# Performance work log

Hardware: AMD Instinct MI355X
Metric: run time of the kernel (lower is better)

Reference implementation:

```python
import jax, jax.numpy as jnp
import numpy as np

HEADS = 8
DIM_HEAD = 64


def setup_inputs() -> dict:
    key = jax.random.key(0)
    k1, k2, k3 = jax.random.split(key, 3)
    dim = 512
    hidden = HEADS * DIM_HEAD  # 512
    x = jax.random.normal(k1, (16, dim, 64, 64), dtype=jnp.float32)
    # 1x1 convs are matmuls over channels; store weights as [out_ch, in_ch]
    w_qkv = jax.random.normal(k2, (3 * hidden, dim), dtype=jnp.float32) * (1.0 / np.sqrt(dim))
    w_out = jax.random.normal(k3, (dim, hidden), dtype=jnp.float32) * (1.0 / np.sqrt(hidden))
    b_out = jnp.zeros((dim,), dtype=jnp.float32)
    return {"x": x, "w_qkv": w_qkv, "w_out": w_out, "b_out": b_out}


def reference(x, w_qkv, w_out, b_out):
    b, c, h, w = x.shape
    n = h * w
    xf = x.reshape(b, c, n)                          # [b, c, n]
    qkv = jnp.einsum('oc,bcn->bon', w_qkv, xf)        # 1x1 conv, no bias -> [b, 3*H*D, n]
    qkv = qkv.reshape(b, 3, HEADS, DIM_HEAD, n)       # split (qkv heads c)
    q, k, v = qkv[:, 0], qkv[:, 1], qkv[:, 2]         # each [b, H, D, n]
    k = jax.nn.softmax(k, axis=-1)                    # softmax over spatial tokens
    context = jnp.einsum('bhdn,bhen->bhde', k, v)     # [b, H, D, D]
    out = jnp.einsum('bhde,bhdn->bhen', context, q)   # [b, H, D, n]
    out = out.reshape(b, HEADS * DIM_HEAD, n)
    out = jnp.einsum('oc,bcn->bon', w_out, out) + b_out[None, :, None]  # 1x1 conv + bias
    return out.reshape(b, -1, h, w)
```

## Files before the change

### kernel.cpp

```cpp
#include <hip/hip_runtime.h>
#include <hip/hip_bf16.h>
#include <math.h>


typedef __attribute__((ext_vector_type(8))) __bf16 bf16x8;
typedef __attribute__((ext_vector_type(4))) float f32x4;

__device__ inline void async_ld16(const void* g, void* s) {
    __builtin_amdgcn_global_load_lds(
        (const __attribute__((address_space(1))) void*)g,
        (__attribute__((address_space(3))) void*)s, 16, 0, 0);
}

template<bool OUTBF, bool BIAS>
__global__ __launch_bounds__(256) void gemm_mfma(
    const __bf16* __restrict__ A, const __bf16* __restrict__ BT,
    void* __restrict__ Cv, const float* __restrict__ bias,
    int K, int N, long aBS, long bBS, long cBS)
{
    __shared__ __bf16 As[128 * 32];
    __shared__ __bf16 Bs[128 * 32];

    const int t = threadIdx.x;
    const int lane = t & 63, wv = t >> 6;
    const int z = blockIdx.z;
    const int row0 = blockIdx.y * 128, col0 = blockIdx.x * 128;

    A  += (long)z * aBS;
    BT += (long)z * bBS;

    const int wm = (wv >> 1) * 64, wn = (wv & 1) * 64;
    const int lr = lane & 15, kg = lane >> 4;

    f32x4 acc[4][4] = {};

    const int srow = (lane >> 2);
    const int skk  = (lane & 3) * 8;

    for (int k0 = 0; k0 < K; k0 += 32) {
        #pragma unroll
        for (int it = 0; it < 2; it++) {
            int c = it * 4 + wv;
            int r = c * 16 + srow;
            async_ld16(A  + (long)(row0 + r) * K + k0 + skk, &As[c * 512 + lane * 8]);
            async_ld16(BT + (long)(col0 + r) * K + k0 + skk, &Bs[c * 512 + lane * 8]);
        }
        __syncthreads();

        bf16x8 af[4], bfr[4];
        #pragma unroll
        for (int i = 0; i < 4; i++) {
            af[i]  = *(const bf16x8*)&As[(wm + i * 16 + lr) * 32 + kg * 8];
            bfr[i] = *(const bf16x8*)&Bs[(wn + i * 16 + lr) * 32 + kg * 8];
        }
        #pragma unroll
        for (int i = 0; i < 4; i++)
            #pragma unroll
            for (int j = 0; j < 4; j++)
                acc[i][j] = __builtin_amdgcn_mfma_f32_16x16x32_bf16(af[i], bfr[j], acc[i][j], 0, 0, 0);
        __syncthreads();
    }

    #pragma unroll
    for (int i = 0; i < 4; i++) {
        #pragma unroll
        for (int j = 0; j < 4; j++) {
            #pragma unroll
            for (int r = 0; r < 4; r++) {
                int row = row0 + wm + i * 16 + kg * 4 + r;
                int col = col0 + wn + j * 16 + lr;
                float v = acc[i][j][r];
                if (OUTBF) {
                    ((__hip_bfloat16*)Cv)[(long)z * cBS + (long)row * N + col] = __float2bfloat16(v);
                } else {
                    if (BIAS) v += bias[row];
                    ((float*)Cv)[(long)z * cBS + (long)row * N + col] = v;
                }
            }
        }
    }
}

__global__ __launch_bounds__(256) void transpose_cast(
    const float* __restrict__ x, __hip_bfloat16* __restrict__ xT)
{
    __shared__ float tile[32][33];
    int z = blockIdx.z;
    int n0 = blockIdx.x * 32, c0 = blockIdx.y * 32;
    int tx = threadIdx.x & 31, ty = threadIdx.x >> 5;

    const float* xb = x + (long)z * 512 * 4096;
    #pragma unroll
    for (int i = 0; i < 4; i++)
        tile[ty + i * 8][tx] = xb[(long)(c0 + ty + i * 8) * 4096 + n0 + tx];
    __syncthreads();

    __hip_bfloat16* xTb = xT + (long)z * 4096 * 512;
    #pragma unroll
    for (int i = 0; i < 4; i++) {
        int nl = ty + i * 8;
        xTb[(long)(n0 + nl) * 512 + c0 + tx] = __float2bfloat16(tile[tx][nl]);
    }
}

__global__ __launch_bounds__(256) void cast_bf(
    const float* __restrict__ in, __hip_bfloat16* __restrict__ out, int n)
{
    for (int i = blockIdx.x * 256 + threadIdx.x; i < n; i += gridDim.x * 256)
        out[i] = __float2bfloat16(in[i]);
}

__global__ __launch_bounds__(256) void softmax_bf(__hip_bfloat16* __restrict__ kv)
{
    int b = blockIdx.x >> 9;
    int r = blockIdx.x & 511;
    unsigned short* row = (unsigned short*)(kv + ((long)b * 1024 + r) * 4096);

    int t = threadIdx.x, lane = t & 63, wv = t >> 6;
    __shared__ float red[8];

    float vals[16];
    float m = -INFINITY;
    #pragma unroll
    for (int i = 0; i < 2; i++) {
        uint4 raw = *(const uint4*)&row[8 * t + 2048 * i];
        unsigned v[4] = {raw.x, raw.y, raw.z, raw.w};
        #pragma unroll
        for (int j = 0; j < 4; j++) {
            float lo = __uint_as_float(v[j] << 16);
            float hi = __uint_as_float(v[j] & 0xffff0000u);
            vals[i * 8 + j * 2]     = lo;
            vals[i * 8 + j * 2 + 1] = hi;
            m = fmaxf(m, fmaxf(lo, hi));
        }
    }
    #pragma unroll
    for (int off = 32; off > 0; off >>= 1) m = fmaxf(m, __shfl_down(m, off));
    if (lane == 0) red[wv] = m;
    __syncthreads();
    if (t == 0) red[0] = fmaxf(fmaxf(red[0], red[1]), fmaxf(red[2], red[3]));
    __syncthreads();
    m = red[0];

    float s = 0.0f;
    #pragma unroll
    for (int i = 0; i < 16; i++) { vals[i] = __expf(vals[i] - m); s += vals[i]; }
    #pragma unroll
    for (int off = 32; off > 0; off >>= 1) s += __shfl_down(s, off);
    if (lane == 0) red[4 + wv] = s;
    __syncthreads();
    if (t == 0) red[4] = red[4] + red[5] + red[6] + red[7];
    __syncthreads();
    float inv = 1.0f / red[4];

    #pragma unroll
    for (int i = 0; i < 2; i++) {
        unsigned v[4];
        #pragma unroll
        for (int j = 0; j < 4; j++) {
            __hip_bfloat16 lo = __float2bfloat16(vals[i * 8 + j * 2] * inv);
            __hip_bfloat16 hi = __float2bfloat16(vals[i * 8 + j * 2 + 1] * inv);
            v[j] = (unsigned)(*(unsigned short*)&lo) | ((unsigned)(*(unsigned short*)&hi) << 16);
        }
        uint4 o; o.x = v[0]; o.y = v[1]; o.z = v[2]; o.w = v[3];
        *(uint4*)&row[8 * t + 2048 * i] = o;
    }
}

template<bool BF16>
__device__ inline float ldg_cvt(const float* p, long i) {
    if (BF16) return __bfloat162float(((const __hip_bfloat16*)p)[i]);
    return p[i];
}

template<bool TRANSB, bool BIAS, int MODE, bool BF16IN>
__global__ __launch_bounds__(256) void gemm64(
    const float* __restrict__ A, const float* __restrict__ Bm,
    float* __restrict__ Cm, const float* __restrict__ bias,
    int M, int Nn, int K, int ldA, int ldB, int ldC,
    long aBS, long bBS, long cBS)
{
    const int t  = threadIdx.x;
    const int tx = t & 15;
    const int ty = t >> 4;
    const int z  = blockIdx.z;

    int row0 = blockIdx.y * 64;
    int col0 = blockIdx.x * 64;

    long aBase = 0, bBase = 0, cBase = 0;
    if (MODE == 0) {
        aBase = z * aBS; bBase = z * bBS; cBase = z * cBS;
    } else if (MODE == 1) {
        int bh = z >> 3, ks = z & 7;
        int b = bh >> 3, h = bh & 7;
        aBase = ((long)b * 1024 + h * 64) * 4096 + ks * 512;
        bBase = ((long)b * 1024 + 512 + h * 64) * 4096 + ks * 512;
        cBase = (long)z * 4096;
    } else {
        aBase = (long)(z & 7) * 64;
        bBase = (long)z * 4096;
        cBase = (long)(z >> 3) * 262144 + (long)(z & 7) * 64;
    }

    __shared__ __align__(16) float As[16][68];
    __shared__ __align__(16) float Bs[16][68];

    float acc[4][4] = {};

    for (int k0 = 0; k0 < K; k0 += 16) {
        {
            int k = t & 15, r = t >> 4;
            #pragma unroll
            for (int i = 0; i < 4; i++)
                As[k][r + i * 16] = ldg_cvt<BF16IN>(A, aBase + (long)(row0 + r + i * 16) * ldA + k0 + k);
        }
        if (TRANSB) {
            int k = t & 15, c = t >> 4;
            #pragma unroll
            for (int i = 0; i < 4; i++)
                Bs[k][c + i * 16] = ldg_cvt<BF16IN>(Bm, bBase + (long)(col0 + c + i * 16) * ldB + k0 + k);
        } else {
            int c = t & 63, kq = t >> 6;
            #pragma unroll
            for (int i = 0; i < 4; i++)
                Bs[kq + i * 4][c] = ldg_cvt<BF16IN>(Bm, bBase + (long)(k0 + kq + i * 4) * ldB + col0 + c);
        }
        __syncthreads();

        #pragma unroll
        for (int kk = 0; kk < 16; kk++) {
            float4 a4 = *(const float4*)&As[kk][ty * 4];
            float4 b4 = *(const float4*)&Bs[kk][tx * 4];
            float av[4] = {a4.x, a4.y, a4.z, a4.w};
            float bv[4] = {b4.x, b4.y, b4.z, b4.w};
            #pragma unroll
            for (int i = 0; i < 4; i++)
                #pragma unroll
                for (int j = 0; j < 4; j++)
                    acc[i][j] = fmaf(av[i], bv[j], acc[i][j]);
        }
        __syncthreads();
    }

    #pragma unroll
    for (int i = 0; i < 4; i++) {
        int r = row0 + ty * 4 + i;
        float bv = BIAS ? bias[r] : 0.0f;
        float4 o;
        o.x = acc[i][0] + bv; o.y = acc[i][1] + bv;
        o.z = acc[i][2] + bv; o.w = acc[i][3] + bv;
        *(float4*)&Cm[cBase + (long)r * ldC + col0 + tx * 4] = o;
    }
}

__global__ __launch_bounds__(256) void reduce_ctx(
    const float* __restrict__ part, float* __restrict__ ctx)
{
    int bh = blockIdx.x;
    for (int i = threadIdx.x; i < 4096; i += 256) {
        float s = 0.0f;
        #pragma unroll
        for (int ks = 0; ks < 8; ks++)
            s += part[((long)bh * 8 + ks) * 4096 + i];
        ctx[(long)bh * 4096 + i] = s;
    }
}

extern "C" void kernel_launch(void* const* d_in, const int* in_sizes, int n_in,
                              void* d_out, int out_size, void* d_ws, size_t ws_size,
                              hipStream_t stream)
{
    const float* x     = (const float*)d_in[0];
    const float* w_qkv = (const float*)d_in[1];
    const float* w_out = (const float*)d_in[2];
    const float* b_out = (const float*)d_in[3];
    float* out = (float*)d_out;

    char* ws = (char*)d_ws;
    __hip_bfloat16* kv_bf  = (__hip_bfloat16*)(ws);
    __hip_bfloat16* xT     = (__hip_bfloat16*)(ws + 134217728L);
    float*          ctxp   = (float*)(ws + 201326592L);
    float*          ctx    = (float*)(ws + 218103808L);
    float*          w2     = (float*)(ws + 220200960L);
    float*          w3     = (float*)(ws + 236978176L);
    __hip_bfloat16* w3bf   = (__hip_bfloat16*)(ws + 253755392L);
    __hip_bfloat16* wkvbf  = (__hip_bfloat16*)(ws + 262144000L);

    transpose_cast<<<dim3(128, 16, 16), 256, 0, stream>>>(x, xT);
    cast_bf<<<dim3(512), 256, 0, stream>>>(w_qkv + 512 * 512, wkvbf, 1024 * 512);

    gemm_mfma<true, false><<<dim3(32, 8, 16), 256, 0, stream>>>(
        (const __bf16*)wkvbf, (const __bf16*)xT, kv_bf, nullptr,
        512, 4096, 0L, (long)4096 * 512, (long)1024 * 4096);

    softmax_bf<<<dim3(8192), 256, 0, stream>>>(kv_bf);

    gemm64<true, false, 1, true><<<dim3(1, 1, 1024), 256, 0, stream>>>(
        (const float*)kv_bf, (const float*)kv_bf, ctxp, nullptr,
        64, 64, 512, 4096, 4096, 64, 0L, 0L, 0L);
    reduce_ctx<<<dim3(128), 256, 0, stream>>>(ctxp, ctx);

    gemm64<true, false, 2, false><<<dim3(1, 8, 128), 256, 0, stream>>>(
        w_out, ctx, w2, nullptr,
        512, 64, 64, 512, 64, 512, 0L, 0L, 0L);

    gemm64<false, false, 0, false><<<dim3(8, 8, 16), 256, 0, stream>>>(
        w2, w_qkv, w3, nullptr,
        512, 512, 512, 512, 512, 512,
        262144L, 0L, 262144L);
    cast_bf<<<dim3(512), 256, 0, stream>>>(w3, w3bf, 16 * 512 * 512);

    gemm_mfma<false, true><<<dim3(32, 4, 16), 256, 0, stream>>>(
        (const __bf16*)w3bf, (const __bf16*)xT, out, b_out,
        512, 4096, (long)512 * 512, (long)4096 * 512, (long)512 * 4096);
}
```

Baseline: 584.8 us.

## Fuse softmax normalization into MFMA context kernel and move weight-fold GEMM to MFMA

Splits the softmax into a row-stats pass that writes only max and inverse sum. The exp and normalization are then recomputed inside a new MFMA-based context kernel, which removes the write-back of normalized K. The scalar fp32 w2·w_qkv fold GEMM is replaced by a bf16 MFMA GEMM using a transposed bf16 copy of the Q weights, and its output is written as bf16 directly, dropping the separate cast pass. This adds an extra weight transpose kernel and recomputes exp once per element. It also lowers the precision of the intermediate w2 and w3.

```diff
diff --git a/kernel.cpp b/kernel.cpp
--- a/kernel.cpp
+++ b/kernel.cpp
@@ -103,6 +103,21 @@
     }
 }
 
+__global__ __launch_bounds__(256) void transpose_cast_sq(
+    const float* __restrict__ in, __hip_bfloat16* __restrict__ out)
+{
+    __shared__ float tile[32][33];
+    int r0 = blockIdx.y * 32, c0 = blockIdx.x * 32;
+    int tx = threadIdx.x & 31, ty = threadIdx.x >> 5;
+    #pragma unroll
+    for (int i = 0; i < 4; i++)
+        tile[ty + i * 8][tx] = in[(long)(r0 + ty + i * 8) * 512 + c0 + tx];
+    __syncthreads();
+    #pragma unroll
+    for (int i = 0; i < 4; i++)
+        out[(long)(c0 + ty + i * 8) * 512 + r0 + tx] = __float2bfloat16(tile[tx][ty + i * 8]);
+}
+
 __global__ __launch_bounds__(256) void cast_bf(
     const float* __restrict__ in, __hip_bfloat16* __restrict__ out, int n)
 {
@@ -110,11 +125,12 @@
         out[i] = __float2bfloat16(in[i]);
 }
 
-__global__ __launch_bounds__(256) void softmax_bf(__hip_bfloat16* __restrict__ kv)
+__global__ __launch_bounds__(256) void row_stats(
+    const __hip_bfloat16* __restrict__ kv, float2* __restrict__ stats)
 {
     int b = blockIdx.x >> 9;
     int r = blockIdx.x & 511;
-    unsigned short* row = (unsigned short*)(kv + ((long)b * 1024 + r) * 4096);
+    const unsigned short* row = (const unsigned short*)(kv + ((long)b * 1024 + r) * 4096);
 
     int t = threadIdx.x, lane = t & 63, wv = t >> 6;
     __shared__ float red[8];
@@ -144,41 +160,92 @@
 
     float s = 0.0f;
     #pragma unroll
-    for (int i = 0; i < 16; i++) { vals[i] = __expf(vals[i] - m); s += vals[i]; }
+    for (int i = 0; i < 16; i++) s += __expf(vals[i] - m);
     #pragma unroll
     for (int off = 32; off > 0; off >>= 1) s += __shfl_down(s, off);
     if (lane == 0) red[4 + wv] = s;
     __syncthreads();
-    if (t == 0) red[4] = red[4] + red[5] + red[6] + red[7];
-    __syncthreads();
-    float inv = 1.0f / red[4];
-
-    #pragma unroll
-    for (int i = 0; i < 2; i++) {
-        unsigned v[4];
+    if (t == 0) {
+        float stot = red[4] + red[5] + red[6] + red[7];
+        stats[blockIdx.x] = make_float2(m, 1.0f / stot);
+    }
+}
+
+__global__ __launch_bounds__(256) void ctx_mfma(
+    const __hip_bfloat16* __restrict__ kv, const float2* __restrict__ stats,
+    float* __restrict__ part)
+{
+    int ks = blockIdx.x, bh = blockIdx.y;
+    int b = bh >> 3, h = bh & 7;
+    const __hip_bfloat16* Krow = kv + ((long)b * 1024 + h * 64) * 4096 + ks * 512;
+    const __hip_bfloat16* Vrow = kv + ((long)b * 1024 + 512 + h * 64) * 4096 + ks * 512;
+
+    __shared__ __bf16 Ps[64 * 32];
+    __shared__ __bf16 Vs[64 * 32];
+
+    int t = threadIdx.x, lane = t & 63, wv = t >> 6;
+    int lr = lane & 15, kg = lane >> 4;
+
+    int prow = t >> 2, pc = (t & 3) * 8;
+    float2 s2 = stats[b * 512 + h * 64 + prow];
+    float pm = s2.x, pinv = s2.y;
+
+    f32x4 acc[4] = {};
+
+    for (int k0 = 0; k0 < 512; k0 += 32) {
+        {
+            int vrow = wv * 16 + (lane >> 2);
+            int vc   = (lane & 3) * 8;
+            async_ld16(Vrow + (long)vrow * 4096 + k0 + vc, &Vs[wv * 16 * 32 + lane * 8]);
+        }
+        {
+            uint4 raw = *(const uint4*)(Krow + (long)prow * 4096 + k0 + pc);
+            unsigned v[4] = {raw.x, raw.y, raw.z, raw.w};
+            __hip_bfloat16 pb[8];
+            #pragma unroll
+            for (int j = 0; j < 4; j++) {
+                float lo = __uint_as_float(v[j] << 16);
+                float hi = __uint_as_float(v[j] & 0xffff0000u);
+                pb[j * 2]     = __float2bfloat16(__expf(lo - pm) * pinv);
+                pb[j * 2 + 1] = __float2bfloat16(__expf(hi - pm) * pinv);
+            }
+            *(bf16x8*)&Ps[prow * 32 + pc] = *(const bf16x8*)pb;
+        }
+        __syncthreads();
+
+        bf16x8 af = *(const bf16x8*)&Ps[(wv * 16 + lr) * 32 + kg * 8];
         #pragma unroll
         for (int j = 0; j < 4; j++) {
-            __hip_bfloat16 lo = __float2bfloat16(vals[i * 8 + j * 2] * inv);
-            __hip_bfloat16 hi = __float2bfloat16(vals[i * 8 + j * 2 + 1] * inv);
-            v[j] = (unsigned)(*(unsigned short*)&lo) | ((unsigned)(*(unsigned short*)&hi) << 16);
-        }
-        uint4 o; o.x = v[0]; o.y = v[1]; o.z = v[2]; o.w = v[3];
-        *(uint4*)&row[8 * t + 2048 * i] = o;
-    }
-}
-
-template<bool BF16>
-__device__ inline float ldg_cvt(const float* p, long i) {
-    if (BF16) return __bfloat162float(((const __hip_bfloat16*)p)[i]);
-    return p[i];
-}
-
-template<bool TRANSB, bool BIAS, int MODE, bool BF16IN>
-__global__ __launch_bounds__(256) void gemm64(
+            bf16x8 bfr = *(const bf16x8*)&Vs[(j * 16 + lr) * 32 + kg * 8];
+            acc[j] = __builtin_amdgcn_mfma_f32_16x16x32_bf16(af, bfr, acc[j], 0, 0, 0);
+        }
+        __syncthreads();
+    }
+
+    float* P = part + ((long)bh * 8 + ks) * 4096;
+    #pragma unroll
+    for (int j = 0; j < 4; j++)
+        #pragma unroll
+        for (int r = 0; r < 4; r++)
+            P[(wv * 16 + kg * 4 + r) * 64 + j * 16 + lr] = acc[j][r];
+}
+
+__global__ __launch_bounds__(256) void reduce_ctx(
+    const float* __restrict__ part, float* __restrict__ ctx)
+{
+    int bh = blockIdx.x;
+    for (int i = threadIdx.x; i < 4096; i += 256) {
+        float s = 0.0f;
+        #pragma unroll
+        for (int ks = 0; ks < 8; ks++)
+            s += part[((long)bh * 8 + ks) * 4096 + i];
+        ctx[(long)bh * 4096 + i] = s;
+    }
+}
+
+__global__ __launch_bounds__(256) void gemm64_w2(
     const float* __restrict__ A, const float* __restrict__ Bm,
-    float* __restrict__ Cm, const float* __restrict__ bias,
-    int M, int Nn, int K, int ldA, int ldB, int ldC,
-    long aBS, long bBS, long cBS)
+    __hip_bfloat16* __restrict__ Cb)
 {
     const int t  = threadIdx.x;
     const int tx = t & 15;
@@ -186,45 +253,28 @@
     const int z  = blockIdx.z;
 
     int row0 = blockIdx.y * 64;
-    int col0 = blockIdx.x * 64;
-
-    long aBase = 0, bBase = 0, cBase = 0;
-    if (MODE == 0) {
-        aBase = z * aBS; bBase = z * bBS; cBase = z * cBS;
-    } else if (MODE == 1) {
-        int bh = z >> 3, ks = z & 7;
-        int b = bh >> 3, h = bh & 7;
-        aBase = ((long)b * 1024 + h * 64) * 4096 + ks * 512;
-        bBase = ((long)b * 1024 + 512 + h * 64) * 4096 + ks * 512;
-        cBase = (long)z * 4096;
-    } else {
-        aBase = (long)(z & 7) * 64;
-        bBase = (long)z * 4096;
-        cBase = (long)(z >> 3) * 262144 + (long)(z & 7) * 64;
-    }
+
+    long aBase = (long)(z & 7) * 64;
+    long bBase = (long)z * 4096;
+    long cBase = (long)(z >> 3) * 262144 + (long)(z & 7) * 64;
 
     __shared__ __align__(16) float As[16][68];
     __shared__ __align__(16) float Bs[16][68];
 
     float acc[4][4] = {};
 
-    for (int k0 = 0; k0 < K; k0 += 16) {
+    for (int k0 = 0; k0 < 64; k0 += 16) {
         {
             int k = t & 15, r = t >> 4;
             #pragma unroll
             for (int i = 0; i < 4; i++)
-                As[k][r + i * 16] = ldg_cvt<BF16IN>(A, aBase + (long)(row0 + r + i * 16) * ldA + k0 + k);
-        }
-        if (TRANSB) {
+                As[k][r + i * 16] = A[aBase + (long)(row0 + r + i * 16) * 512 + k0 + k];
+        }
+        {
             int k = t & 15, c = t >> 4;
             #pragma unroll
             for (int i = 0; i < 4; i++)
-                Bs[k][c + i * 16] = ldg_cvt<BF16IN>(Bm, bBase + (long)(col0 + c + i * 16) * ldB + k0 + k);
-        } else {
-            int c = t & 63, kq = t >> 6;
-            #pragma unroll
-            for (int i = 0; i < 4; i++)
-                Bs[kq + i * 4][c] = ldg_cvt<BF16IN>(Bm, bBase + (long)(k0 + kq + i * 4) * ldB + col0 + c);
+                Bs[k][c + i * 16] = Bm[bBase + (long)(c + i * 16) * 64 + k0 + k];
         }
         __syncthreads();
 
@@ -246,24 +296,10 @@
     #pragma unroll
     for (int i = 0; i < 4; i++) {
         int r = row0 + ty * 4 + i;
-        float bv = BIAS ? bias[r] : 0.0f;
-        float4 o;
-        o.x = acc[i][0] + bv; o.y = acc[i][1] + bv;
-        o.z = acc[i][2] + bv; o.w = acc[i][3] + bv;
-        *(float4*)&Cm[cBase + (long)r * ldC + col0 + tx * 4] = o;
-    }
-}
-
-__global__ __launch_bounds__(256) void reduce_ctx(
-    const float* __restrict__ part, float* __restrict__ ctx)
-{
-    int bh = blockIdx.x;
-    for (int i = threadIdx.x; i < 4096; i += 256) {
-        float s = 0.0f;
-        #pragma unroll
-        for (int ks = 0; ks < 8; ks++)
-            s += part[((long)bh * 8 + ks) * 4096 + i];
-        ctx[(long)bh * 4096 + i] = s;
+        __hip_bfloat16 o4[4];
+        #pragma unroll
+        for (int j = 0; j < 4; j++) o4[j] = __float2bfloat16(acc[i][j]);
+        *(short4*)&Cb[cBase + (long)r * 512 + tx * 4] = *(const short4*)o4;
     }
 }
 
@@ -282,34 +318,30 @@
     __hip_bfloat16* xT     = (__hip_bfloat16*)(ws + 134217728L);
     float*          ctxp   = (float*)(ws + 201326592L);
     float*          ctx    = (float*)(ws + 218103808L);
-    float*          w2     = (float*)(ws + 220200960L);
-    float*          w3     = (float*)(ws + 236978176L);
-    __hip_bfloat16* w3bf   = (__hip_bfloat16*)(ws + 253755392L);
-    __hip_bfloat16* wkvbf  = (__hip_bfloat16*)(ws + 262144000L);
+    __hip_bfloat16* w2bf   = (__hip_bfloat16*)(ws + 220200960L);
+    __hip_bfloat16* w3bf   = (__hip_bfloat16*)(ws + 228589568L);
+    __hip_bfloat16* wkvbf  = (__hip_bfloat16*)(ws + 236978176L);
+    __hip_bfloat16* wqT    = (__hip_bfloat16*)(ws + 238026752L);
+    float2*         stats  = (float2*)(ws + 238551040L);
 
     transpose_cast<<<dim3(128, 16, 16), 256, 0, stream>>>(x, xT);
     cast_bf<<<dim3(512), 256, 0, stream>>>(w_qkv + 512 * 512, wkvbf, 1024 * 512);
+    transpose_cast_sq<<<dim3(16, 16), 256, 0, stream>>>(w_qkv, wqT);
 
     gemm_mfma<true, false><<<dim3(32, 8, 16), 256, 0, stream>>>(
         (const __bf16*)wkvbf, (const __bf16*)xT, kv_bf, nullptr,
         512, 4096, 0L, (long)4096 * 512, (long)1024 * 4096);
 
-    softmax_bf<<<dim3(8192), 256, 0, stream>>>(kv_bf);
-
-    gemm64<true, false, 1, true><<<dim3(1, 1, 1024), 256, 0, stream>>>(
-        (const float*)kv_bf, (const float*)kv_bf, ctxp, nullptr,
-        64, 64, 512, 4096, 4096, 64, 0L, 0L, 0L);
+    row_stats<<<dim3(8192), 256, 0, stream>>>(kv_bf, stats);
+
+    ctx_mfma<<<dim3(8, 128), 256, 0, stream>>>(kv_bf, stats, ctxp);
     reduce_ctx<<<dim3(128), 256, 0, stream>>>(ctxp, ctx);
 
-    gemm64<true, false, 2, false><<<dim3(1, 8, 128), 256, 0, stream>>>(
-        w_out, ctx, w2, nullptr,
-        512, 64, 64, 512, 64, 512, 0L, 0L, 0L);
-
-    gemm64<false, false, 0, false><<<dim3(8, 8, 16), 256, 0, stream>>>(
-        w2, w_qkv, w3, nullptr,
-        512, 512, 512, 512, 512, 512,
-        262144L, 0L, 262144L);
-    cast_bf<<<dim3(512), 256, 0, stream>>>(w3, w3bf, 16 * 512 * 512);
+    gemm64_w2<<<dim3(1, 8, 128), 256, 0, stream>>>(w_out, ctx, w2bf);
+
+    gemm_mfma<true, false><<<dim3(4, 4, 16), 256, 0, stream>>>(
+        (const __bf16*)w2bf, (const __bf16*)wqT, w3bf, nullptr,
+        512, 512, 262144L, 0L, 262144L);
 
     gemm_mfma<false, true><<<dim3(32, 4, 16), 256, 0, stream>>>(
         (const __bf16*)w3bf, (const __bf16*)xT, out, b_out,
```

Measured after the change: 485.6 us. 1.2x faster.
